# Kernel tuning notes

Measured on AMD Instinct MI355X. Metric: run time of the kernel, lower is better.

Reference implementation:

```python
import jax, jax.numpy as jnp
import numpy as np

B, T, E = 4, 2048, 1024
H, D = 16, 64  # n_heads, head_size


def setup_inputs() -> dict:
    key = jax.random.key(0)
    ks = jax.random.split(key, 6)
    s = 0.02
    x = jax.random.normal(ks[0], (B, T, E), dtype=jnp.float32)
    Wq = jax.random.normal(ks[1], (H, E, D), dtype=jnp.float32) * s
    Wk = jax.random.normal(ks[2], (H, E, D), dtype=jnp.float32) * s
    Wv = jax.random.normal(ks[3], (H, E, D), dtype=jnp.float32) * s
    Wp = jax.random.normal(ks[4], (E, E), dtype=jnp.float32) * s
    bp = jnp.zeros((E,), dtype=jnp.float32)
    return {"x": x, "Wq": Wq, "Wk": Wk, "Wv": Wv, "Wp": Wp, "bp": bp}


def reference(x, Wq, Wk, Wv, Wp, bp):
    # Per-head bias-free Q/K/V projections (vectorized over heads)
    q = jnp.einsum('bte,hed->bhtd', x, Wq)
    k = jnp.einsum('bte,hed->bhtd', x, Wk)
    v = jnp.einsum('bte,hed->bhtd', x, Wv)
    scale = 1.0 / jnp.sqrt(jnp.asarray(D, dtype=x.dtype))
    scores = jnp.einsum('bhtd,bhsd->bhts', q, k) * scale  # [B,H,T,T]
    causal = jnp.tril(jnp.ones((T, T), dtype=bool))
    scores = jnp.where(causal, scores, jnp.asarray(-jnp.inf, dtype=scores.dtype))
    attn = jax.nn.softmax(scores, axis=-1)
    out = jnp.einsum('bhts,bhsd->bhtd', attn, v)  # [B,H,T,D]
    # concat heads: 'nh b t c -> b t (nh c)'
    out = out.transpose(0, 2, 1, 3).reshape(B, T, H * D)
    # output projection (dropout p=0.0 is identity)
    return out @ Wp.T + bp
```

## Files before the change

kernel.cpp:

```cpp
#include <hip/hip_runtime.h>

typedef unsigned short u16;
typedef __attribute__((ext_vector_type(8))) short bf16x8;
typedef __attribute__((ext_vector_type(4))) short bf16x4;
typedef __attribute__((ext_vector_type(4))) float f32x4;

__device__ __forceinline__ u16 f2bf(float f) {
  unsigned u = __float_as_uint(f);
  u += 0x7FFFu + ((u >> 16) & 1u);
  return (u16)(u >> 16);
}
__device__ __forceinline__ unsigned pack2(float a, float b) {
  return (unsigned)f2bf(a) | ((unsigned)f2bf(b) << 16);
}
#if __has_builtin(__builtin_amdgcn_cvt_pk_bf16_f32)
typedef __attribute__((ext_vector_type(2))) __bf16 bf16v2;
__device__ __forceinline__ unsigned cvt_pk(float a, float b) {
  bf16v2 v = __builtin_amdgcn_cvt_pk_bf16_f32(a, b);
  return __builtin_bit_cast(unsigned, v);
}
#else
__device__ __forceinline__ unsigned cvt_pk(float a, float b) { return pack2(a, b); }
#endif
__device__ __forceinline__ uint4 pack8(float4 a, float4 b) {
  uint4 r;
  r.x = cvt_pk(a.x, a.y); r.y = cvt_pk(a.z, a.w);
  r.z = cvt_pk(b.x, b.y); r.w = cvt_pk(b.z, b.w);
  return r;
}
__device__ __forceinline__ void gload16(const void* g, void* l) {
  __builtin_amdgcn_global_load_lds(
      (const __attribute__((address_space(1))) void*)g,
      (__attribute__((address_space(3))) void*)l, 16, 0, 0);
}
__device__ __forceinline__ f32x4 mfma16(bf16x4 a, bf16x4 b, f32x4 c) {
#if __has_builtin(__builtin_amdgcn_mfma_f32_16x16x16bf16_1k)
  return __builtin_amdgcn_mfma_f32_16x16x16bf16_1k(a, b, c, 0, 0, 0);
#elif __has_builtin(__builtin_amdgcn_mfma_f32_16x16x16_bf16)
  return __builtin_amdgcn_mfma_f32_16x16x16_bf16(a, b, c, 0, 0, 0);
#else
  asm volatile("v_mfma_f32_16x16x16_bf16 %0, %1, %2, %0\n\ts_nop 2"
               : "+v"(c) : "v"(a), "v"(b));
  return c;
#endif
}

__global__ __launch_bounds__(256) void prep(
    const float* __restrict__ x, u16* __restrict__ xbf,
    const float* __restrict__ Wq, const float* __restrict__ Wk,
    const float* __restrict__ Wv, u16* __restrict__ wt,
    const float* __restrict__ Wp, u16* __restrict__ wpbf) {
  const int tid = threadIdx.x;
  const int b = blockIdx.x;
  __shared__ __align__(16) u16 tile[64 * 72];
  if (b < 4096) {
    const size_t i = (size_t)b * 256 + tid;
    const float4* p = (const float4*)(x + i * 8);
    *(uint4*)(xbf + i * 8) = pack8(p[0], p[1]);
  } else if (b < 4864) {
    const int idx = b - 4096;
    const int w = idx >> 8;
    const int mat = (idx >> 4) & 15;
    const int r0 = (idx & 15) * 64;
    const float* src = (w == 0 ? Wq : (w == 1 ? Wk : Wv)) + (size_t)mat * 1024 * 64;
    u16* dst = wt + (size_t)w * 1024 * 1024 + (size_t)mat * 1024 * 64;
#pragma unroll
    for (int i = 0; i < 2; ++i) {
      const int c = tid + i * 256;
      const int r = c >> 3, off = (c & 7) * 8;
      const float* p = src + (size_t)(r0 + r) * 64 + off;
      *(uint4*)(&tile[r * 72 + off]) = pack8(*(const float4*)p, *(const float4*)(p + 4));
    }
    __syncthreads();
#pragma unroll
    for (int i = 0; i < 2; ++i) {
      const int c = tid + i * 256;
      const int d = c >> 3, roff = (c & 7) * 8;
      bf16x8 v;
#pragma unroll
      for (int j = 0; j < 8; ++j) v[j] = (short)tile[(roff + j) * 72 + d];
      *(bf16x8*)(dst + (size_t)d * 1024 + r0 + roff) = v;
    }
  } else {
    const size_t i = (size_t)(b - 4864) * 256 + tid;
    const float4* p = (const float4*)(Wp + i * 8);
    *(uint4*)(wpbf + i * 8) = pack8(p[0], p[1]);
  }
}

template <int MODE>
__global__ __launch_bounds__(256) void gemm_bt(
    const u16* __restrict__ A, const u16* __restrict__ BT,
    u16* __restrict__ o0, u16* __restrict__ o1, u16* __restrict__ o2,
    float* __restrict__ fout, const float* __restrict__ bp) {
  __shared__ __align__(16) u16 As[2][128 * 32];
  __shared__ __align__(16) u16 Bs[2][128 * 32];
  const int tid = threadIdx.x;
  const int lane = tid & 63, wv = tid >> 6;
  const int g = lane >> 4, ln = lane & 15;
  const int wm = wv >> 1, wn = wv & 1;
  const int m0 = blockIdx.x * 128, n0 = blockIdx.y * 128;

  const f32x4 fz = {0.f, 0.f, 0.f, 0.f};
  f32x4 acc[4][4];
#pragma unroll
  for (int i = 0; i < 4; ++i)
#pragma unroll
    for (int j = 0; j < 4; ++j) acc[i][j] = fz;

  for (int k0 = 0; k0 < 1024; k0 += 64) {
    __syncthreads();
#pragma unroll
    for (int hf = 0; hf < 2; ++hf)
#pragma unroll
      for (int j = 0; j < 2; ++j) {
        const int c = j * 256 + tid;
        const int r = c >> 2, off = (c & 3) * 8;
        gload16(A + (size_t)(m0 + r) * 1024 + k0 + hf * 32 + off, &As[hf][c * 8]);
        gload16(BT + (size_t)(n0 + r) * 1024 + k0 + hf * 32 + off, &Bs[hf][c * 8]);
      }
    __syncthreads();
#pragma unroll
    for (int hf = 0; hf < 2; ++hf) {
      bf16x8 af[4], bfr[4];
#pragma unroll
      for (int rt = 0; rt < 4; ++rt)
        af[rt] = *(const bf16x8*)(&As[hf][(wm * 64 + rt * 16 + ln) * 32 + g * 8]);
#pragma unroll
      for (int ct = 0; ct < 4; ++ct)
        bfr[ct] = *(const bf16x8*)(&Bs[hf][(wn * 64 + ct * 16 + ln) * 32 + g * 8]);
#pragma unroll
      for (int rt = 0; rt < 4; ++rt)
#pragma unroll
        for (int ct = 0; ct < 4; ++ct)
          acc[rt][ct] = __builtin_amdgcn_mfma_f32_16x16x32_bf16(af[rt], bfr[ct],
                                                                acc[rt][ct], 0, 0, 0);
    }
  }

  if (MODE == 0) {
    const int which = n0 >> 10;
    const int nl0 = (n0 & 1023) + wn * 64;
    const float qs = (which == 0) ? 0.1803368801f : 1.0f;
    if (which < 2) {
#pragma unroll
      for (int rt = 0; rt < 4; ++rt)
#pragma unroll
        for (int ct = 0; ct < 4; ++ct) {
          const int nl = nl0 + ct * 16 + ln;
          const int h = nl >> 6, d = nl & 63;
          const unsigned p01 = cvt_pk(acc[rt][ct][0] * qs, acc[rt][ct][1] * qs);
          const unsigned p23 = cvt_pk(acc[rt][ct][2] * qs, acc[rt][ct][3] * qs);
          const u16 vv[4] = {(u16)p01, (u16)(p01 >> 16), (u16)p23, (u16)(p23 >> 16)};
#pragma unroll
          for (int r = 0; r < 4; ++r) {
            const int m = m0 + wm * 64 + rt * 16 + 4 * g + r;
            const int b = m >> 11, t = m & 2047;
            const size_t bh_base = (size_t)(b * 16 + h) * 131072;
            if (which == 0) {
              o0[bh_base + (size_t)t * 64 + d] = vv[r];
            } else {
              o1[bh_base + (size_t)(t >> 6) * 4096 + (d >> 3) * 512 +
                 (t & 63) * 8 + (d & 7)] = vv[r];
            }
          }
        }
    } else {
#pragma unroll
      for (int rt = 0; rt < 4; ++rt) {
        const int tb = m0 + wm * 64 + rt * 16 + 4 * g;
        const int b = tb >> 11, t = tb & 2047;
        const int tile = t >> 6, tl = t & 63;
#pragma unroll
        for (int ct = 0; ct < 4; ++ct) {
          const int nl = nl0 + ct * 16 + ln;
          const int h = nl >> 6, d = nl & 63;
          uint2 pv;
          pv.x = cvt_pk(acc[rt][ct][0], acc[rt][ct][1]);
          pv.y = cvt_pk(acc[rt][ct][2], acc[rt][ct][3]);
          *(uint2*)(o2 + (size_t)(b * 16 + h) * 131072 + (size_t)tile * 4096 +
                    (tl >> 3) * 512 + d * 8 + ((tl >> 2) & 1) * 4) = pv;
        }
      }
    }
  } else {
#pragma unroll
    for (int ct = 0; ct < 4; ++ct) {
      const int n = n0 + wn * 64 + ct * 16 + ln;
      const float bias = bp[n];
#pragma unroll
      for (int rt = 0; rt < 4; ++rt)
#pragma unroll
        for (int r = 0; r < 4; ++r) {
          const int m = m0 + wm * 64 + rt * 16 + 4 * g + r;
          fout[(size_t)m * 1024 + n] = acc[rt][ct][r] + bias;
        }
    }
  }
}

__global__ __launch_bounds__(256) void attn_kernel(
    const u16* __restrict__ Q, const u16* __restrict__ K,
    const u16* __restrict__ VT, u16* __restrict__ AO) {
  const int tid = threadIdx.x;
  const int wv = tid >> 6, lane = tid & 63, g = lane >> 4, ln = lane & 15;
  const int bh = blockIdx.x;
  const int qi = 15 - blockIdx.y;
  const u16* Qb = Q + (size_t)bh * 131072;
  const u16* Kb = K + (size_t)bh * 131072;
  const u16* Vb = VT + (size_t)bh * 131072;

  __shared__ __align__(16) u16 KV[3][2][4096];

  const int b = bh >> 4, h = bh & 15;
  const short ob = 0x3F80;
  const bf16x4 ones = {ob, ob, ob, ob};
  const f32x4 fz = {0.f, 0.f, 0.f, 0.f};

  const int q0 = qi * 128;
  const int nt = 2 * qi + 2;
  const int ntw = 2 * qi + 1 + (wv >> 1);

  const int L0 = tid, L1 = tid + 256;

  bf16x8 qa[2][2];
#pragma unroll
  for (int rt = 0; rt < 2; ++rt) {
    const int row = q0 + wv * 32 + rt * 16 + ln;
#pragma unroll
    for (int hh = 0; hh < 2; ++hh)
      qa[rt][hh] = *(const bf16x8*)(Qb + (size_t)row * 64 + hh * 32 + g * 8);
  }

#define STAGE(buf, tile)                                              \
  {                                                                   \
    const u16* kt_ = Kb + (size_t)(tile) * 4096;                      \
    const u16* vt_ = Vb + (size_t)(tile) * 4096;                      \
    gload16(kt_ + L0 * 8, &KV[buf][0][L0 * 8]);                       \
    gload16(kt_ + L1 * 8, &KV[buf][0][L1 * 8]);                       \
    gload16(vt_ + L0 * 8, &KV[buf][1][L0 * 8]);                       \
    gload16(vt_ + L1 * 8, &KV[buf][1][L1 * 8]);                       \
  }

  STAGE(0, 0);
  STAGE(1, 1);

  f32x4 oacc[2][4], lacc[2];
#pragma unroll
  for (int rt = 0; rt < 2; ++rt) {
    lacc[rt] = fz;
#pragma unroll
    for (int dt = 0; dt < 4; ++dt) oacc[rt][dt] = fz;
  }

  for (int kt = 0; kt < nt; ++kt) {
    __builtin_amdgcn_s_barrier();
    __builtin_amdgcn_sched_barrier(0);
    if (kt + 2 < nt) {
      STAGE((kt + 2) % 3, kt + 2);
      asm volatile("s_waitcnt vmcnt(8)" ::: "memory");
    } else if (kt + 1 < nt) {
      asm volatile("s_waitcnt vmcnt(4)" ::: "memory");
    } else {
      asm volatile("s_waitcnt vmcnt(0)" ::: "memory");
    }
    __builtin_amdgcn_sched_barrier(0);
    __builtin_amdgcn_s_barrier();
    __builtin_amdgcn_sched_barrier(0);
    if (kt < ntw) {
      const int bufi = kt % 3;
      const u16* Ksb = &KV[bufi][0][0];
      const u16* Vsb = &KV[bufi][1][0];
      const int s0 = kt * 64;
      f32x4 sfT[2][4];
#pragma unroll
      for (int st = 0; st < 4; ++st) {
        const bf16x8 kb0 = *(const bf16x8*)(Ksb + (g * 64 + st * 16 + ln) * 8);
        const bf16x8 kb1 =
            *(const bf16x8*)(Ksb + ((g + 4) * 64 + st * 16 + ln) * 8);
#pragma unroll
        for (int rt = 0; rt < 2; ++rt) {
          sfT[rt][st] = __builtin_amdgcn_mfma_f32_16x16x32_bf16(kb0, qa[rt][0],
                                                                fz, 0, 0, 0);
          sfT[rt][st] = __builtin_amdgcn_mfma_f32_16x16x32_bf16(kb1, qa[rt][1],
                                                                sfT[rt][st], 0, 0, 0);
        }
      }
      const bool diag = (kt == ntw - 1);
      bf16x4 pa[2][4];
#pragma unroll
      for (int rt = 0; rt < 2; ++rt) {
        const int qloc = wv * 32 + rt * 16 + ln;
#pragma unroll
        for (int st = 0; st < 4; ++st) {
          float e[4];
#pragma unroll
          for (int r = 0; r < 4; ++r) e[r] = __builtin_amdgcn_exp2f(sfT[rt][st][r]);
          if (diag) {
            const int sloc = s0 - q0 + st * 16 + 4 * g;
#pragma unroll
            for (int r = 0; r < 4; ++r)
              if (sloc + r > qloc) e[r] = 0.f;
          }
          uint2 packed = {cvt_pk(e[0], e[1]), cvt_pk(e[2], e[3])};
          pa[rt][st] = __builtin_bit_cast(bf16x4, packed);
        }
      }
#pragma unroll
      for (int st = 0; st < 4; ++st) {
#pragma unroll
        for (int dt = 0; dt < 4; ++dt) {
          const bf16x4 vb = *(const bf16x4*)(
              Vsb + ((st * 2 + (g >> 1)) * 64 + dt * 16 + ln) * 8 + (g & 1) * 4);
#pragma unroll
          for (int rt = 0; rt < 2; ++rt)
            oacc[rt][dt] = mfma16(pa[rt][st], vb, oacc[rt][dt]);
        }
#pragma unroll
        for (int rt = 0; rt < 2; ++rt)
          lacc[rt] = mfma16(pa[rt][st], ones, lacc[rt]);
      }
    }
  }
#undef STAGE
#pragma unroll
  for (int rt = 0; rt < 2; ++rt) {
    float linv[4];
#pragma unroll
    for (int r = 0; r < 4; ++r) linv[r] = 1.f / lacc[rt][r];
#pragma unroll
    for (int dt = 0; dt < 4; ++dt) {
      const unsigned p01 =
          cvt_pk(oacc[rt][dt][0] * linv[0], oacc[rt][dt][1] * linv[1]);
      const unsigned p23 =
          cvt_pk(oacc[rt][dt][2] * linv[2], oacc[rt][dt][3] * linv[3]);
      const u16 vv[4] = {(u16)p01, (u16)(p01 >> 16), (u16)p23, (u16)(p23 >> 16)};
#pragma unroll
      for (int r = 0; r < 4; ++r) {
        const int qg = q0 + wv * 32 + rt * 16 + 4 * g + r;
        AO[(size_t)(b * 2048 + qg) * 1024 + h * 64 + dt * 16 + ln] = vv[r];
      }
    }
  }
}

extern "C" void kernel_launch(void* const* d_in, const int* in_sizes, int n_in,
                              void* d_out, int out_size, void* d_ws, size_t ws_size,
                              hipStream_t stream) {
  const float* x  = (const float*)d_in[0];
  const float* Wq = (const float*)d_in[1];
  const float* Wk = (const float*)d_in[2];
  const float* Wv = (const float*)d_in[3];
  const float* Wp = (const float*)d_in[4];
  const float* bp = (const float*)d_in[5];
  float* out = (float*)d_out;

  char* ws = (char*)d_ws;
  const size_t MB = 1048576;
  u16* xbf  = (u16*)(ws);
  u16* aows = (u16*)(ws);
  u16* wt   = (u16*)(ws + 16 * MB);
  u16* wpbf = (u16*)(ws + 22 * MB);
  u16* qws  = (u16*)(ws + 24 * MB);
  u16* kws  = (u16*)(ws + 40 * MB);
  u16* vtws = (u16*)(ws + 56 * MB);

  prep<<<dim3(5376), 256, 0, stream>>>(x, xbf, Wq, Wk, Wv, wt, Wp, wpbf);
  gemm_bt<0><<<dim3(64, 24), 256, 0, stream>>>(xbf, wt, qws, kws, vtws,
                                               nullptr, nullptr);
  attn_kernel<<<dim3(64, 16), 256, 0, stream>>>(qws, kws, vtws, aows);
  gemm_bt<1><<<dim3(64, 8), 256, 0, stream>>>(aows, wpbf, nullptr, nullptr,
                                              nullptr, out, bp);
}
```

Measured before the change: 266.3 us.

## Process two K/V tiles per barrier step with double buffering and MFMA priority

The attention loop now stages pairs of 64-key tiles into a double-buffered shared-memory array, replacing the triple-buffered single-tile pipeline. This halves the number of barrier/wait iterations and batches the QK MFMAs, exp/pack work, and PV MFMAs across two tiles. s_setprio is raised around the MFMA phases to favour matrix issue across waves. LDS use grows (64KB vs 48KB), which may reduce occupancy, and register pressure rises from the doubled sfT/pa arrays. Prefetch depth in tiles stays at two, but the granularity is coarser.

```diff
diff --git a/kernel.cpp b/kernel.cpp
--- a/kernel.cpp
+++ b/kernel.cpp
@@ -210,7 +210,7 @@
   const u16* Kb = K + (size_t)bh * 131072;
   const u16* Vb = VT + (size_t)bh * 131072;
 
-  __shared__ __align__(16) u16 KV[3][2][4096];
+  __shared__ __align__(16) u16 KV[2][2][2][4096];
 
   const int b = bh >> 4, h = bh & 15;
   const short ob = 0x3F80;
@@ -219,6 +219,7 @@
 
   const int q0 = qi * 128;
   const int nt = 2 * qi + 2;
+  const int NW = nt >> 1;
   const int ntw = 2 * qi + 1 + (wv >> 1);
 
   const int L0 = tid, L1 = tid + 256;
@@ -232,18 +233,21 @@
       qa[rt][hh] = *(const bf16x8*)(Qb + (size_t)row * 64 + hh * 32 + g * 8);
   }
 
-#define STAGE(buf, tile)                                              \
+#define STAGE(buf, w_)                                                \
   {                                                                   \
-    const u16* kt_ = Kb + (size_t)(tile) * 4096;                      \
-    const u16* vt_ = Vb + (size_t)(tile) * 4096;                      \
-    gload16(kt_ + L0 * 8, &KV[buf][0][L0 * 8]);                       \
-    gload16(kt_ + L1 * 8, &KV[buf][0][L1 * 8]);                       \
-    gload16(vt_ + L0 * 8, &KV[buf][1][L0 * 8]);                       \
-    gload16(vt_ + L1 * 8, &KV[buf][1][L1 * 8]);                       \
+    const u16* ka_ = Kb + (size_t)(2 * (w_)) * 4096;                  \
+    const u16* va_ = Vb + (size_t)(2 * (w_)) * 4096;                  \
+    gload16(ka_ + L0 * 8, &KV[buf][0][0][L0 * 8]);                    \
+    gload16(ka_ + L1 * 8, &KV[buf][0][0][L1 * 8]);                    \
+    gload16(va_ + L0 * 8, &KV[buf][0][1][L0 * 8]);                    \
+    gload16(va_ + L1 * 8, &KV[buf][0][1][L1 * 8]);                    \
+    gload16(ka_ + 4096 + L0 * 8, &KV[buf][1][0][L0 * 8]);             \
+    gload16(ka_ + 4096 + L1 * 8, &KV[buf][1][0][L1 * 8]);             \
+    gload16(va_ + 4096 + L0 * 8, &KV[buf][1][1][L0 * 8]);             \
+    gload16(va_ + 4096 + L1 * 8, &KV[buf][1][1][L1 * 8]);             \
   }
 
   STAGE(0, 0);
-  STAGE(1, 1);
 
   f32x4 oacc[2][4], lacc[2];
 #pragma unroll
@@ -253,74 +257,94 @@
     for (int dt = 0; dt < 4; ++dt) oacc[rt][dt] = fz;
   }
 
-  for (int kt = 0; kt < nt; ++kt) {
+  for (int w = 0; w < NW; ++w) {
     __builtin_amdgcn_s_barrier();
     __builtin_amdgcn_sched_barrier(0);
-    if (kt + 2 < nt) {
-      STAGE((kt + 2) % 3, kt + 2);
+    if (w + 1 < NW) {
+      STAGE((w + 1) & 1, w + 1);
       asm volatile("s_waitcnt vmcnt(8)" ::: "memory");
-    } else if (kt + 1 < nt) {
-      asm volatile("s_waitcnt vmcnt(4)" ::: "memory");
     } else {
       asm volatile("s_waitcnt vmcnt(0)" ::: "memory");
     }
     __builtin_amdgcn_sched_barrier(0);
     __builtin_amdgcn_s_barrier();
     __builtin_amdgcn_sched_barrier(0);
-    if (kt < ntw) {
-      const int bufi = kt % 3;
-      const u16* Ksb = &KV[bufi][0][0];
-      const u16* Vsb = &KV[bufi][1][0];
-      const int s0 = kt * 64;
-      f32x4 sfT[2][4];
-#pragma unroll
-      for (int st = 0; st < 4; ++st) {
-        const bf16x8 kb0 = *(const bf16x8*)(Ksb + (g * 64 + st * 16 + ln) * 8);
-        const bf16x8 kb1 =
-            *(const bf16x8*)(Ksb + ((g + 4) * 64 + st * 16 + ln) * 8);
+    const int cur = w & 1;
+
+    f32x4 sfT[2][2][4];
+    __builtin_amdgcn_s_setprio(1);
+#pragma unroll
+    for (int hf = 0; hf < 2; ++hf) {
+      if (2 * w + hf < ntw) {
+        const u16* Ksb = &KV[cur][hf][0][0];
+#pragma unroll
+        for (int st = 0; st < 4; ++st) {
+          const bf16x8 kb0 = *(const bf16x8*)(Ksb + (g * 64 + st * 16 + ln) * 8);
+          const bf16x8 kb1 =
+              *(const bf16x8*)(Ksb + ((g + 4) * 64 + st * 16 + ln) * 8);
+#pragma unroll
+          for (int rt = 0; rt < 2; ++rt) {
+            sfT[hf][rt][st] = __builtin_amdgcn_mfma_f32_16x16x32_bf16(
+                kb0, qa[rt][0], fz, 0, 0, 0);
+            sfT[hf][rt][st] = __builtin_amdgcn_mfma_f32_16x16x32_bf16(
+                kb1, qa[rt][1], sfT[hf][rt][st], 0, 0, 0);
+          }
+        }
+      }
+    }
+    __builtin_amdgcn_s_setprio(0);
+
+    bf16x4 pa[2][2][4];
+#pragma unroll
+    for (int hf = 0; hf < 2; ++hf) {
+      const int kt = 2 * w + hf;
+      if (kt < ntw) {
+        const bool diag = (kt == ntw - 1);
+        const int s0 = kt * 64;
 #pragma unroll
         for (int rt = 0; rt < 2; ++rt) {
-          sfT[rt][st] = __builtin_amdgcn_mfma_f32_16x16x32_bf16(kb0, qa[rt][0],
-                                                                fz, 0, 0, 0);
-          sfT[rt][st] = __builtin_amdgcn_mfma_f32_16x16x32_bf16(kb1, qa[rt][1],
-                                                                sfT[rt][st], 0, 0, 0);
-        }
-      }
-      const bool diag = (kt == ntw - 1);
-      bf16x4 pa[2][4];
-#pragma unroll
-      for (int rt = 0; rt < 2; ++rt) {
-        const int qloc = wv * 32 + rt * 16 + ln;
+          const int qloc = wv * 32 + rt * 16 + ln;
+#pragma unroll
+          for (int st = 0; st < 4; ++st) {
+            float e[4];
+#pragma unroll
+            for (int r = 0; r < 4; ++r)
+              e[r] = __builtin_amdgcn_exp2f(sfT[hf][rt][st][r]);
+            if (diag) {
+              const int sloc = s0 - q0 + st * 16 + 4 * g;
+#pragma unroll
+              for (int r = 0; r < 4; ++r)
+                if (sloc + r > qloc) e[r] = 0.f;
+            }
+            uint2 packed = {cvt_pk(e[0], e[1]), cvt_pk(e[2], e[3])};
+            pa[hf][rt][st] = __builtin_bit_cast(bf16x4, packed);
+          }
+        }
+      }
+    }
+
+    __builtin_amdgcn_s_setprio(1);
+#pragma unroll
+    for (int hf = 0; hf < 2; ++hf) {
+      if (2 * w + hf < ntw) {
+        const u16* Vsb = &KV[cur][hf][1][0];
 #pragma unroll
         for (int st = 0; st < 4; ++st) {
-          float e[4];
-#pragma unroll
-          for (int r = 0; r < 4; ++r) e[r] = __builtin_amdgcn_exp2f(sfT[rt][st][r]);
-          if (diag) {
-            const int sloc = s0 - q0 + st * 16 + 4 * g;
-#pragma unroll
-            for (int r = 0; r < 4; ++r)
-              if (sloc + r > qloc) e[r] = 0.f;
+#pragma unroll
+          for (int dt = 0; dt < 4; ++dt) {
+            const bf16x4 vb = *(const bf16x4*)(
+                Vsb + ((st * 2 + (g >> 1)) * 64 + dt * 16 + ln) * 8 + (g & 1) * 4);
+#pragma unroll
+            for (int rt = 0; rt < 2; ++rt)
+              oacc[rt][dt] = mfma16(pa[hf][rt][st], vb, oacc[rt][dt]);
           }
-          uint2 packed = {cvt_pk(e[0], e[1]), cvt_pk(e[2], e[3])};
-          pa[rt][st] = __builtin_bit_cast(bf16x4, packed);
-        }
-      }
-#pragma unroll
-      for (int st = 0; st < 4; ++st) {
-#pragma unroll
-        for (int dt = 0; dt < 4; ++dt) {
-          const bf16x4 vb = *(const bf16x4*)(
-              Vsb + ((st * 2 + (g >> 1)) * 64 + dt * 16 + ln) * 8 + (g & 1) * 4);
 #pragma unroll
           for (int rt = 0; rt < 2; ++rt)
-            oacc[rt][dt] = mfma16(pa[rt][st], vb, oacc[rt][dt]);
-        }
-#pragma unroll
-        for (int rt = 0; rt < 2; ++rt)
-          lacc[rt] = mfma16(pa[rt][st], ones, lacc[rt]);
-      }
-    }
+            lacc[rt] = mfma16(pa[hf][rt][st], ones, lacc[rt]);
+        }
+      }
+    }
+    __builtin_amdgcn_s_setprio(0);
   }
 #undef STAGE
 #pragma unroll
```

Measured after the change: 293.4 us. 1.1x slower.
